# Kernel optimization log

Measured on AMD Instinct MI355X. Metric: run time of the kernel, lower is better.

Reference implementation:

```python
import jax, jax.numpy as jnp
import numpy as np

EPS = 1e-8  # torch F.cosine_similarity denominator clamp


def setup_inputs() -> dict:
    key = jax.random.key(0)
    k1, k2 = jax.random.split(key)
    N, D = 8192, 256
    return {
        "output1": jax.random.normal(k1, (N, D), dtype=jnp.float32),
        "output2": jax.random.normal(k2, (N, D), dtype=jnp.float32),
    }


def reference(output1, output2):
    N = output2.shape[0]
    # cosine similarity matrix via normalize + GEMM, with torch's eps clamp
    n1 = jnp.linalg.norm(output1, axis=-1, keepdims=True)  # [N,1]
    n2 = jnp.linalg.norm(output2, axis=-1, keepdims=True)  # [N,1]
    dots = output1 @ output2.T  # [N,N]
    denom = jnp.maximum(n1 * n2.T, EPS)
    cos = dots / denom
    # subtract tiny diagonal as in original
    cos = cos - jnp.eye(N, dtype=cos.dtype) * 1e-12
    # cross entropy with labels = arange(N)
    logZ = jax.nn.logsumexp(cos, axis=-1)  # [N]
    diag = jnp.diagonal(cos)  # logits at true label i
    loss = jnp.mean(logZ - diag)
    return loss
```

## Files before the change

### kernel.cpp

```cpp
#include <hip/hip_runtime.h>
#include <hip/hip_bf16.h>

#define N 8192
#define D 256
#define SP 8
#define NCHK 16

typedef __bf16 bf16x8 __attribute__((ext_vector_type(8)));
typedef float f32x16 __attribute__((ext_vector_type(16)));

static __device__ __forceinline__ unsigned short f2bf(float x) {
    union { float f; unsigned int u; } c; c.f = x;
    unsigned int r = (c.u + 0x7fffu + ((c.u >> 16) & 1u)) >> 16;
    return (unsigned short)r;
}

static __device__ __forceinline__ void gll16(const void* g, void* l) {
    __builtin_amdgcn_global_load_lds(
        (const __attribute__((address_space(1))) void*)g,
        (__attribute__((address_space(3))) void*)l, 16, 0, 0);
}

#define WAIT_VM4  asm volatile("s_waitcnt vmcnt(4)" ::: "memory")
#define WAIT_VM0  asm volatile("s_waitcnt vmcnt(0)" ::: "memory")
#define WAIT_LG0  asm volatile("s_waitcnt lgkmcnt(0)" ::: "memory")
#define SBAR      __builtin_amdgcn_s_barrier()
#define SCHED0    __builtin_amdgcn_sched_barrier(0)

__global__ __launch_bounds__(256) void conv_k(const float* __restrict__ o1,
                                              const float* __restrict__ o2,
                                              unsigned char* __restrict__ a_bf,
                                              unsigned char* __restrict__ b_bf,
                                              float* __restrict__ diag) {
    const int wid = threadIdx.x >> 6, lane = threadIdx.x & 63;
    const int r = blockIdx.x * 4 + wid;
    const float4* p1 = (const float4*)(o1 + (size_t)r * D);
    const float4* p2 = (const float4*)(o2 + (size_t)r * D);
    float4 v1 = p1[lane], v2 = p2[lane];
    float s1 = v1.x*v1.x + v1.y*v1.y + v1.z*v1.z + v1.w*v1.w;
    float s2 = v2.x*v2.x + v2.y*v2.y + v2.z*v2.z + v2.w*v2.w;
    float sd = v1.x*v2.x + v1.y*v2.y + v1.z*v2.z + v1.w*v2.w;
    #pragma unroll
    for (int m = 1; m < 64; m <<= 1) {
        s1 += __shfl_xor(s1, m);
        s2 += __shfl_xor(s2, m);
        sd += __shfl_xor(sd, m);
    }
    float i1 = 1.0f / sqrtf(s1);
    float i2 = 1.0f / sqrtf(s2);
    if (lane == 0) diag[r] = sd * i1 * i2;

    {
        unsigned int lo = (unsigned int)f2bf(v1.x * i1) | ((unsigned int)f2bf(v1.y * i1) << 16);
        unsigned int hi = (unsigned int)f2bf(v1.z * i1) | ((unsigned int)f2bf(v1.w * i1) << 16);
        uint2 q; q.x = lo; q.y = hi;
        *(uint2*)(a_bf + (size_t)r * 512 + lane * 8) = q;
    }
    {
        unsigned int lo = (unsigned int)f2bf(v2.x * i2) | ((unsigned int)f2bf(v2.y * i2) << 16);
        unsigned int hi = (unsigned int)f2bf(v2.z * i2) | ((unsigned int)f2bf(v2.w * i2) << 16);
        int c  = lane >> 1;
        int cs = c ^ (r & 31);
        uint2 q; q.x = lo; q.y = hi;
        *(uint2*)(b_bf + (size_t)r * 512 + cs * 16 + (lane & 1) * 8) = q;
    }
}

__global__ __launch_bounds__(512, 2) void gemm5(const unsigned char* __restrict__ a_bf,
                                                const unsigned char* __restrict__ b_bf,
                                                float* __restrict__ s_part) {
    __shared__ __align__(16) unsigned char bls[3][64 * 512];
    __shared__ float red[2][256];

    const int tid = threadIdx.x;
    const int lane = tid & 63, wid = tid >> 6;
    const int wr = wid >> 1, wc = wid & 1;
    const int l31 = lane & 31, lhi = lane >> 5;
    const int bid = blockIdx.x;
    const int sp = bid & 7, rb = bid >> 3;

    const unsigned char* aG = a_bf + (size_t)rb * (256 * 512);
    const unsigned char* bG = b_bf + (size_t)sp * ((size_t)1024 * 512);

    bf16x8 af0[16], af1[16];
    #pragma unroll
    for (int k = 0; k < 16; ++k) {
        af0[k] = *(const bf16x8*)(aG + (size_t)(wr * 64 + l31) * 512 + k * 32 + lhi * 16);
        af1[k] = *(const bf16x8*)(aG + (size_t)(wr * 64 + 32 + l31) * 512 + k * 32 + lhi * 16);
    }
    #pragma unroll
    for (int it = 0; it < 4; ++it) {
        int x = it * 8192 + tid * 16;
        gll16(bG + x, &bls[0][x]);
    }
    #pragma unroll
    for (int it = 0; it < 4; ++it) {
        int x = it * 8192 + tid * 16;
        gll16(bG + 32768 + x, &bls[1][x]);
    }

    float srow0[16], srow1[16];
    #pragma unroll
    for (int r = 0; r < 16; ++r) { srow0[r] = 0.f; srow1[r] = 0.f; }

    const unsigned char* cur = bls[0];
    const unsigned char* nx1 = bls[1];
    const unsigned char* stg = bls[2];

    #pragma unroll 1
    for (int p = 0; p < NCHK; ++p) {
        if (p < NCHK - 1) { WAIT_VM4; } else { WAIT_VM0; }
        SCHED0;
        SBAR;

        if (p < NCHK - 2) {
            const unsigned char* src = bG + (size_t)(p + 2) * 32768;
            #pragma unroll
            for (int it = 0; it < 4; ++it) {
                int x = it * 8192 + tid * 16;
                gll16(src + x, (unsigned char*)stg + x);
            }
        }

        f32x16 acc0, acc1;
        #pragma unroll
        for (int r = 0; r < 16; ++r) { acc0[r] = 0.f; acc1[r] = 0.f; }

        __builtin_amdgcn_s_setprio(1);
        #pragma unroll
        for (int ksi = 0; ksi < 16; ++ksi) {
            const int cs = (ksi * 2 + lhi) ^ l31;
            bf16x8 bb = *(const bf16x8*)(cur + (wc * 32 + l31) * 512 + cs * 16);
            acc0 = __builtin_amdgcn_mfma_f32_32x32x16_bf16(af0[ksi], bb, acc0, 0, 0, 0);
            acc1 = __builtin_amdgcn_mfma_f32_32x32x16_bf16(af1[ksi], bb, acc1, 0, 0, 0);
        }
        __builtin_amdgcn_s_setprio(0);
        WAIT_LG0;
        SCHED0;

        #pragma unroll
        for (int r = 0; r < 16; ++r) {
            srow0[r] += __expf(acc0[r]);
            srow1[r] += __expf(acc1[r]);
        }

        const unsigned char* t = cur; cur = nx1; nx1 = stg; stg = t;
    }

    #pragma unroll
    for (int r = 0; r < 16; ++r) {
        float v0 = srow0[r], v1 = srow1[r];
        #pragma unroll
        for (int m = 1; m < 32; m <<= 1) {
            v0 += __shfl_xor(v0, m);
            v1 += __shfl_xor(v1, m);
        }
        srow0[r] = v0; srow1[r] = v1;
    }
    if (l31 == 0) {
        #pragma unroll
        for (int r = 0; r < 16; ++r) {
            int rl = wr * 64 + 4 * lhi + (r & 3) + 8 * (r >> 2);
            red[wc][rl]      = srow0[r];
            red[wc][rl + 32] = srow1[r];
        }
    }
    __syncthreads();
    if (tid < 256) {
        s_part[(size_t)sp * N + rb * 256 + tid] = red[0][tid] + red[1][tid];
    }
}

__global__ __launch_bounds__(128) void rowloss3(const float* __restrict__ s_part,
                                                const float* __restrict__ diag,
                                                float* __restrict__ partial) {
    const int t = threadIdx.x, rb = blockIdx.x;
    float s = 0.f;
    #pragma unroll
    for (int sp = 0; sp < SP; ++sp)
        s += s_part[(size_t)sp * N + rb * 128 + t];
    float loss = logf(s) - diag[rb * 128 + t];
    #pragma unroll
    for (int m = 1; m < 64; m <<= 1) loss += __shfl_xor(loss, m);
    __shared__ float redl[2];
    if ((t & 63) == 0) redl[t >> 6] = loss;
    __syncthreads();
    if (t == 0) partial[rb] = redl[0] + redl[1];
}

__global__ __launch_bounds__(64) void final_k(const float* __restrict__ partial,
                                              float* __restrict__ out) {
    const int t = threadIdx.x;
    float v = partial[t];
    #pragma unroll
    for (int m = 1; m < 64; m <<= 1) v += __shfl_xor(v, m);
    if (t == 0) out[0] = v / (float)N;
}

extern "C" void kernel_launch(void* const* d_in, const int* in_sizes, int n_in,
                              void* d_out, int out_size, void* d_ws, size_t ws_size,
                              hipStream_t stream) {
    const float* o1 = (const float*)d_in[0];
    const float* o2 = (const float*)d_in[1];

    unsigned char* w = (unsigned char*)d_ws;
    unsigned char* a_bf = w;
    unsigned char* b_bf = w + (size_t)4 * 1024 * 1024;
    float* diag    = (float*)(w + (size_t)8 * 1024 * 1024);
    float* s_part  = diag + N;
    float* partial = s_part + (size_t)SP * N;

    conv_k<<<N / 4, 256, 0, stream>>>(o1, o2, a_bf, b_bf, diag);
    gemm5<<<256, 512, 0, stream>>>(a_bf, b_bf, s_part);
    rowloss3<<<N / 128, 128, 0, stream>>>(s_part, diag, partial);
    final_k<<<1, 64, 0, stream>>>(partial, (float*)d_out);
}
```

Baseline: 57.24 us.

## Switch GEMM to 16x16x32 MFMA with per-wave 32-row tiles across all columns

The GEMM kernel moves from 32x32x16 MFMAs on a 2x2-ish wave grid to 16x16x32 MFMAs where each of 8 waves owns 32 rows and covers all 64 columns of a B chunk. This removes the cross-wave LDS reduction and the final __syncthreads, and shortens the row-sum shuffle reduction to 16 lanes. In exchange each wave reads the whole B chunk from LDS (4 fragments per k-step), which raises LDS read traffic per MFMA. The exp count and the register footprint of the A fragments stay about the same.

```diff
diff --git a/kernel.cpp b/kernel.cpp
--- a/kernel.cpp
+++ b/kernel.cpp
@@ -7,7 +7,7 @@
 #define NCHK 16
 
 typedef __bf16 bf16x8 __attribute__((ext_vector_type(8)));
-typedef float f32x16 __attribute__((ext_vector_type(16)));
+typedef float f32x4 __attribute__((ext_vector_type(4)));
 
 static __device__ __forceinline__ unsigned short f2bf(float x) {
     union { float f; unsigned int u; } c; c.f = x;
@@ -66,28 +66,28 @@
     }
 }
 
-__global__ __launch_bounds__(512, 2) void gemm5(const unsigned char* __restrict__ a_bf,
+__global__ __launch_bounds__(512, 2) void gemm6(const unsigned char* __restrict__ a_bf,
                                                 const unsigned char* __restrict__ b_bf,
                                                 float* __restrict__ s_part) {
     __shared__ __align__(16) unsigned char bls[3][64 * 512];
-    __shared__ float red[2][256];
 
     const int tid = threadIdx.x;
     const int lane = tid & 63, wid = tid >> 6;
-    const int wr = wid >> 1, wc = wid & 1;
-    const int l31 = lane & 31, lhi = lane >> 5;
+    const int l15 = lane & 15, lk = lane >> 4;
     const int bid = blockIdx.x;
     const int sp = bid & 7, rb = bid >> 3;
 
     const unsigned char* aG = a_bf + (size_t)rb * (256 * 512);
     const unsigned char* bG = b_bf + (size_t)sp * ((size_t)1024 * 512);
 
-    bf16x8 af0[16], af1[16];
-    #pragma unroll
-    for (int k = 0; k < 16; ++k) {
-        af0[k] = *(const bf16x8*)(aG + (size_t)(wr * 64 + l31) * 512 + k * 32 + lhi * 16);
-        af1[k] = *(const bf16x8*)(aG + (size_t)(wr * 64 + 32 + l31) * 512 + k * 32 + lhi * 16);
-    }
+    bf16x8 af[2][8];
+    #pragma unroll
+    for (int mr = 0; mr < 2; ++mr)
+        #pragma unroll
+        for (int ks = 0; ks < 8; ++ks)
+            af[mr][ks] = *(const bf16x8*)(aG + (size_t)(wid * 32 + mr * 16 + l15) * 512
+                                             + ks * 64 + lk * 16);
+
     #pragma unroll
     for (int it = 0; it < 4; ++it) {
         int x = it * 8192 + tid * 16;
@@ -99,9 +99,11 @@
         gll16(bG + 32768 + x, &bls[1][x]);
     }
 
-    float srow0[16], srow1[16];
-    #pragma unroll
-    for (int r = 0; r < 16; ++r) { srow0[r] = 0.f; srow1[r] = 0.f; }
+    float srow[2][4];
+    #pragma unroll
+    for (int mr = 0; mr < 2; ++mr)
+        #pragma unroll
+        for (int rg = 0; rg < 4; ++rg) srow[mr][rg] = 0.f;
 
     const unsigned char* cur = bls[0];
     const unsigned char* nx1 = bls[1];
@@ -122,52 +124,63 @@
             }
         }
 
-        f32x16 acc0, acc1;
-        #pragma unroll
-        for (int r = 0; r < 16; ++r) { acc0[r] = 0.f; acc1[r] = 0.f; }
+        f32x4 acc[2][4];
+        #pragma unroll
+        for (int mr = 0; mr < 2; ++mr)
+            #pragma unroll
+            for (int nc = 0; nc < 4; ++nc)
+                acc[mr][nc] = (f32x4){0.f, 0.f, 0.f, 0.f};
 
         __builtin_amdgcn_s_setprio(1);
         #pragma unroll
-        for (int ksi = 0; ksi < 16; ++ksi) {
-            const int cs = (ksi * 2 + lhi) ^ l31;
-            bf16x8 bb = *(const bf16x8*)(cur + (wc * 32 + l31) * 512 + cs * 16);
-            acc0 = __builtin_amdgcn_mfma_f32_32x32x16_bf16(af0[ksi], bb, acc0, 0, 0, 0);
-            acc1 = __builtin_amdgcn_mfma_f32_32x32x16_bf16(af1[ksi], bb, acc1, 0, 0, 0);
+        for (int ks = 0; ks < 8; ++ks) {
+            bf16x8 bb[4];
+            #pragma unroll
+            for (int nc = 0; nc < 4; ++nc) {
+                const int col = nc * 16 + l15;
+                const int cs = (ks * 4 + lk) ^ (col & 31);
+                bb[nc] = *(const bf16x8*)(cur + col * 512 + cs * 16);
+            }
+            #pragma unroll
+            for (int nc = 0; nc < 4; ++nc)
+                #pragma unroll
+                for (int mr = 0; mr < 2; ++mr)
+                    acc[mr][nc] = __builtin_amdgcn_mfma_f32_16x16x32_bf16(
+                        af[mr][ks], bb[nc], acc[mr][nc], 0, 0, 0);
         }
         __builtin_amdgcn_s_setprio(0);
         WAIT_LG0;
         SCHED0;
 
         #pragma unroll
-        for (int r = 0; r < 16; ++r) {
-            srow0[r] += __expf(acc0[r]);
-            srow1[r] += __expf(acc1[r]);
+        for (int mr = 0; mr < 2; ++mr)
+            #pragma unroll
+            for (int rg = 0; rg < 4; ++rg)
+                srow[mr][rg] += __expf(acc[mr][0][rg]) + __expf(acc[mr][1][rg])
+                              + __expf(acc[mr][2][rg]) + __expf(acc[mr][3][rg]);
+
+        const unsigned char* t = cur; cur = nx1; nx1 = stg; stg = t;
+    }
+
+    #pragma unroll
+    for (int mr = 0; mr < 2; ++mr)
+        #pragma unroll
+        for (int rg = 0; rg < 4; ++rg) {
+            float v = srow[mr][rg];
+            v += __shfl_xor(v, 1);
+            v += __shfl_xor(v, 2);
+            v += __shfl_xor(v, 4);
+            v += __shfl_xor(v, 8);
+            srow[mr][rg] = v;
         }
-
-        const unsigned char* t = cur; cur = nx1; nx1 = stg; stg = t;
-    }
-
-    #pragma unroll
-    for (int r = 0; r < 16; ++r) {
-        float v0 = srow0[r], v1 = srow1[r];
-        #pragma unroll
-        for (int m = 1; m < 32; m <<= 1) {
-            v0 += __shfl_xor(v0, m);
-            v1 += __shfl_xor(v1, m);
-        }
-        srow0[r] = v0; srow1[r] = v1;
-    }
-    if (l31 == 0) {
-        #pragma unroll
-        for (int r = 0; r < 16; ++r) {
-            int rl = wr * 64 + 4 * lhi + (r & 3) + 8 * (r >> 2);
-            red[wc][rl]      = srow0[r];
-            red[wc][rl + 32] = srow1[r];
-        }
-    }
-    __syncthreads();
-    if (tid < 256) {
-        s_part[(size_t)sp * N + rb * 256 + tid] = red[0][tid] + red[1][tid];
+    if (l15 == 0) {
+        #pragma unroll
+        for (int mr = 0; mr < 2; ++mr)
+            #pragma unroll
+            for (int rg = 0; rg < 4; ++rg) {
+                int row = wid * 32 + mr * 16 + lk * 4 + rg;
+                s_part[(size_t)sp * N + rb * 256 + row] = srow[mr][rg];
+            }
     }
 }
 
@@ -211,7 +224,7 @@
     float* partial = s_part + (size_t)SP * N;
 
     conv_k<<<N / 4, 256, 0, stream>>>(o1, o2, a_bf, b_bf, diag);
-    gemm5<<<256, 512, 0, stream>>>(a_bf, b_bf, s_part);
+    gemm6<<<256, 512, 0, stream>>>(a_bf, b_bf, s_part);
     rowloss3<<<N / 128, 128, 0, stream>>>(s_part, diag, partial);
     final_k<<<1, 64, 0, stream>>>(partial, (float*)d_out);
 }
```

After: 50.90 us. -11.1%, faster.
